# Kernel optimization log

Hardware: AMD Instinct MI355X
Metric: run time of the kernel (lower is better)

The kernel has to match this reference:

```python
import jax, jax.numpy as jnp
import numpy as np

LN_EPS = 1e-5


def setup_inputs() -> dict:
    key = jax.random.key(0)
    ks = jax.random.split(key, 6)
    n_nodes, mem_dim = 500000, 256
    n_upd, msg_dim = 65536, 512
    return {
        "unique_node_ids": jnp.arange(n_upd, dtype=jnp.int64) if jax.config.jax_enable_x64 else jnp.arange(n_upd, dtype=jnp.int32),
        "unique_messages": jax.random.normal(ks[0], (n_upd, msg_dim), dtype=jnp.float32),
        "timestamps": jax.random.uniform(ks[1], (n_upd,), dtype=jnp.float32),
        "memory": jax.random.normal(ks[2], (n_nodes, mem_dim), dtype=jnp.float32),
        "last_update": jnp.zeros((n_nodes,), dtype=jnp.float32),
        "W_ih": jax.random.normal(ks[3], (3 * mem_dim, msg_dim), dtype=jnp.float32) * (1.0 / np.sqrt(msg_dim)),
        "W_hh": jax.random.normal(ks[4], (3 * mem_dim, mem_dim), dtype=jnp.float32) * (1.0 / np.sqrt(mem_dim)),
        "b_ih": jnp.zeros((3 * mem_dim,), dtype=jnp.float32),
        "b_hh": jnp.zeros((3 * mem_dim,), dtype=jnp.float32),
        "ln_gamma": jnp.ones((mem_dim,), dtype=jnp.float32),
        "ln_beta": jnp.zeros((mem_dim,), dtype=jnp.float32),
    }


def _gru_cell(x, h, W_ih, W_hh, b_ih, b_hh):
    # torch.nn.GRUCell math
    gi = x @ W_ih.T + b_ih          # [N, 3H]
    gh = h @ W_hh.T + b_hh          # [N, 3H]
    i_r, i_z, i_n = jnp.split(gi, 3, axis=-1)
    h_r, h_z, h_n = jnp.split(gh, 3, axis=-1)
    r = jax.nn.sigmoid(i_r + h_r)
    z = jax.nn.sigmoid(i_z + h_z)
    n = jnp.tanh(i_n + r * h_n)
    return (1.0 - z) * n + z * h


def _layer_norm(x, gamma, beta):
    mu = jnp.mean(x, axis=-1, keepdims=True)
    var = jnp.mean(jnp.square(x - mu), axis=-1, keepdims=True)
    return (x - mu) * jax.lax.rsqrt(var + LN_EPS) * gamma + beta


def reference(unique_node_ids, unique_messages, timestamps, memory, last_update,
              W_ih, W_hh, b_ih, b_hh, ln_gamma, ln_beta):
    # gather memory rows for the nodes being updated
    h = memory[unique_node_ids]                      # [N, H]
    new_h = _gru_cell(unique_messages, h, W_ih, W_hh, b_ih, b_hh)
    new_h = _layer_norm(new_h, ln_gamma, ln_beta)
    # scatter updated rows back (get_updated_memory semantics: pure copy)
    updated_memory = memory.at[unique_node_ids].set(new_h)
    updated_last_update = last_update.at[unique_node_ids].set(timestamps)
    return updated_memory, updated_last_update
```

## Files before the change

### kernel.cpp

```cpp
#include <hip/hip_runtime.h>
#include <hip/hip_bf16.h>

typedef float  f32x4 __attribute__((ext_vector_type(4)));
typedef short  s16x8 __attribute__((ext_vector_type(8)));

#define MEMH   256
#define MSGD   512
#define G3     768
#define W_IH_ELEMS (G3*MSGD)
#define W_HH_ELEMS (G3*MEMH)
#define W_TOT_ELEMS (W_IH_ELEMS + W_HH_ELEMS)
#define W_BYTES    ((size_t)W_TOT_ELEMS * 2)

#define BM     32
#define NTHR   512
#define AM_OFF 0
#define AH_OFF 32768
#define PART_OFF 49152
#define LDS_BYTES 51200

static __device__ __forceinline__ short f2bf(float x) {
    __hip_bfloat16 b = __float2bfloat16(x);
    return __builtin_bit_cast(short, b);
}
static __device__ __forceinline__ float bf2f(short s) {
    unsigned int u = ((unsigned int)(unsigned short)s) << 16;
    return __builtin_bit_cast(float, u);
}
static __device__ __forceinline__ float sigf(float x) {
    return 1.f / (1.f + __expf(-x));
}
static __device__ __forceinline__ float tanh_fast(float x) {
    float e = __expf(-2.f * fabsf(x));
    float t = (1.f - e) / (1.f + e);
    return copysignf(t, x);
}
static __device__ __forceinline__ f32x4 ntload4(const float* p) {
    return __builtin_nontemporal_load((const f32x4*)p);
}
static __device__ __forceinline__ void ntstore4(float* p, f32x4 v) {
    __builtin_nontemporal_store(v, (f32x4*)p);
}

__global__ void smu_copy_kernel(const float* __restrict__ mem,
                                const float* __restrict__ lu,
                                float* __restrict__ out_mem,
                                float* __restrict__ out_lu,
                                long n_mem4, long n_lu4) {
    long i = (long)blockIdx.x * blockDim.x + threadIdx.x;
    long stride = (long)gridDim.x * blockDim.x;
    long total = n_mem4 + n_lu4;
    for (; i < total; i += stride) {
        if (i < n_mem4) ntstore4(out_mem + i * 4, ntload4(mem + i * 4));
        else {
            long j = (i - n_mem4) * 4;
            ntstore4(out_lu + j, ntload4(lu + j));
        }
    }
}

__global__ __launch_bounds__(256)
void smu_copy_skip_kernel(const float* __restrict__ mem,
                          const float* __restrict__ lu,
                          const unsigned* __restrict__ bm,
                          float* __restrict__ out_mem,
                          float* __restrict__ out_lu,
                          long n_nodes) {
    const long nu = n_nodes * (MEMH / 4);
    const long stride = (long)gridDim.x * blockDim.x;
    const long i0 = (long)blockIdx.x * blockDim.x + threadIdx.x;

    for (long i = i0; i < nu; i += stride) {
        long r = i >> 6;
        if (!((bm[r >> 5] >> (r & 31)) & 1u))
            ntstore4(out_mem + i * 4, ntload4(mem + i * 4));
    }
    for (long i = i0; i < n_nodes; i += stride) {
        if (!((bm[i >> 5] >> (i & 31)) & 1u)) {
            float v = __builtin_nontemporal_load(lu + i);
            __builtin_nontemporal_store(v, out_lu + i);
        }
    }
}

__global__ void smu_cvtw_kernel(const float* __restrict__ wih,
                                const float* __restrict__ whh,
                                short* __restrict__ o) {
    int i = blockIdx.x * blockDim.x + threadIdx.x;
    if (i >= W_TOT_ELEMS) return;
    if (i < W_IH_ELEMS) {
        int f = i >> 9, r = i & 511, l = r >> 3, e = r & 7;
        int t = f >> 4, k = f & 15;
        int row = t * 16 + (l & 15), col = k * 32 + (l >> 4) * 8 + e;
        o[i] = f2bf(wih[row * MSGD + col]);
    } else {
        int j = i - W_IH_ELEMS;
        int f = j >> 9, r = j & 511, l = r >> 3, e = r & 7;
        int t = f >> 3, k = f & 7;
        int row = t * 16 + (l & 15), col = k * 32 + (l >> 4) * 8 + e;
        o[i] = f2bf(whh[row * MEMH + col]);
    }
}

__global__ void smu_clear_kernel(unsigned* __restrict__ p, int n) {
    int i = blockIdx.x * blockDim.x + threadIdx.x;
    if (i < n) p[i] = 0u;
}
__global__ void smu_bits_kernel(const int* __restrict__ ids,
                                unsigned* __restrict__ bm, int n) {
    int i = blockIdx.x * blockDim.x + threadIdx.x;
    if (i < n) {
        int id = ids[i];
        atomicOr(&bm[id >> 5], 1u << (id & 31));
    }
}

template<bool USE_WS>
static __device__ __forceinline__ s16x8 load_b(const float* __restrict__ Wf,
                                               const short* __restrict__ Wb,
                                               int t, int k, int ldk, int nkt, int lane) {
    if constexpr (USE_WS) {
        return *(const s16x8*)(Wb + ((size_t)(t * nkt + k) << 9) + lane * 8);
    } else {
        int row = t * 16 + (lane & 15);
        int col = k * 32 + (lane >> 4) * 8;
        f32x4 x = *(const f32x4*)(Wf + (size_t)row * ldk + col);
        f32x4 y = *(const f32x4*)(Wf + (size_t)row * ldk + col + 4);
        s16x8 s;
        s[0]=f2bf(x[0]); s[1]=f2bf(x[1]); s[2]=f2bf(x[2]); s[3]=f2bf(x[3]);
        s[4]=f2bf(y[0]); s[5]=f2bf(y[1]); s[6]=f2bf(y[2]); s[7]=f2bf(y[3]);
        return s;
    }
}

template<bool USE_WS>
__global__ __launch_bounds__(NTHR, 4)
void smu_gru_kernel(const int*   __restrict__ ids,
                    const float* __restrict__ msg,
                    const float* __restrict__ ts,
                    const float* __restrict__ memory,
                    const float* __restrict__ W_ih,
                    const float* __restrict__ W_hh,
                    const float* __restrict__ b_ih,
                    const float* __restrict__ b_hh,
                    const float* __restrict__ gamma,
                    const float* __restrict__ beta,
                    const short* __restrict__ wsw,
                    float* __restrict__ out_mem,
                    float* __restrict__ out_lu) {
    __shared__ __align__(16) unsigned char lds[LDS_BYTES];
    const int tid = threadIdx.x;
    const long base = (long)blockIdx.x * BM;

    {
        const float* src = msg + base * MSGD;
        #pragma unroll
        for (int it = 0; it < 4; ++it) {
            int u = tid + NTHR * it;
            int row = u >> 6;
            f32x4 a = ntload4(src + u * 8);
            f32x4 b = ntload4(src + u * 8 + 4);
            s16x8 s;
            s[0]=f2bf(a[0]); s[1]=f2bf(a[1]); s[2]=f2bf(a[2]); s[3]=f2bf(a[3]);
            s[4]=f2bf(b[0]); s[5]=f2bf(b[1]); s[6]=f2bf(b[2]); s[7]=f2bf(b[3]);
            int byte = AM_OFF + ((u * 16) ^ ((row & 7) << 4));
            *(s16x8*)(lds + byte) = s;
        }
        #pragma unroll
        for (int it = 0; it < 2; ++it) {
            int u = tid + NTHR * it;
            int row = u >> 5;
            int c8  = u & 31;
            int id  = ids[base + row];
            const float* hs = memory + (size_t)id * MEMH + c8 * 8;
            f32x4 a = ntload4(hs);
            f32x4 b = ntload4(hs + 4);
            s16x8 s;
            s[0]=f2bf(a[0]); s[1]=f2bf(a[1]); s[2]=f2bf(a[2]); s[3]=f2bf(a[3]);
            s[4]=f2bf(b[0]); s[5]=f2bf(b[1]); s[6]=f2bf(b[2]); s[7]=f2bf(b[3]);
            int byte = AH_OFF + ((u * 16) ^ ((row & 7) << 4));
            *(s16x8*)(lds + byte) = s;
        }
    }
    __syncthreads();

    const int lane = tid & 63;
    const int w    = tid >> 6;
    const int lr   = lane & 15;
    const int lk8  = (lane >> 4) * 8;
    const int sw   = (lr & 7) << 4;
    const short* Wi = wsw;
    const short* Wh = wsw + W_IH_ELEMS;

    f32x4 rz[2][2][2] = {};
    f32x4 gin[2][2]   = {};
    f32x4 ghn[2][2]   = {};

    {
        s16x8 b[2][6];
        #pragma unroll
        for (int i = 0; i < 6; ++i)
            b[0][i] = load_b<USE_WS>(W_ih, Wi, w + 8*(i/3) + 16*(i%3), 0, MSGD, 16, lane);
        #pragma unroll
        for (int i = 0; i < 6; ++i)
            b[1][i] = load_b<USE_WS>(W_ih, Wi, w + 8*(i/3) + 16*(i%3), 1, MSGD, 16, lane);
        #pragma unroll
        for (int k = 0; k < 16; ++k) {
            const int cb = (k * 32 + lk8) * 2;
            #pragma unroll
            for (int m = 0; m < 2; ++m) {
                s16x8 a = *(const s16x8*)(lds + AM_OFF + (((m*16 + lr) * 1024 + cb) ^ sw));
                #pragma unroll
                for (int ci = 0; ci < 2; ++ci) {
                    rz[m][ci][0] = __builtin_amdgcn_mfma_f32_16x16x32_bf16(a, b[k & 1][ci*3+0], rz[m][ci][0], 0, 0, 0);
                    rz[m][ci][1] = __builtin_amdgcn_mfma_f32_16x16x32_bf16(a, b[k & 1][ci*3+1], rz[m][ci][1], 0, 0, 0);
                    gin[m][ci]   = __builtin_amdgcn_mfma_f32_16x16x32_bf16(a, b[k & 1][ci*3+2], gin[m][ci],   0, 0, 0);
                }
            }
            if (k < 14) {
                #pragma unroll
                for (int i = 0; i < 6; ++i)
                    b[k & 1][i] = load_b<USE_WS>(W_ih, Wi, w + 8*(i/3) + 16*(i%3), k + 2, MSGD, 16, lane);
            }
        }
    }
    {
        s16x8 b[2][6];
        #pragma unroll
        for (int i = 0; i < 6; ++i)
            b[0][i] = load_b<USE_WS>(W_hh, Wh, w + 8*(i/3) + 16*(i%3), 0, MEMH, 8, lane);
        #pragma unroll
        for (int i = 0; i < 6; ++i)
            b[1][i] = load_b<USE_WS>(W_hh, Wh, w + 8*(i/3) + 16*(i%3), 1, MEMH, 8, lane);
        #pragma unroll
        for (int k = 0; k < 8; ++k) {
            const int cb = (k * 32 + lk8) * 2;
            #pragma unroll
            for (int m = 0; m < 2; ++m) {
                s16x8 a = *(const s16x8*)(lds + AH_OFF + (((m*16 + lr) * 512 + cb) ^ sw));
                #pragma unroll
                for (int ci = 0; ci < 2; ++ci) {
                    rz[m][ci][0] = __builtin_amdgcn_mfma_f32_16x16x32_bf16(a, b[k & 1][ci*3+0], rz[m][ci][0], 0, 0, 0);
                    rz[m][ci][1] = __builtin_amdgcn_mfma_f32_16x16x32_bf16(a, b[k & 1][ci*3+1], rz[m][ci][1], 0, 0, 0);
                    ghn[m][ci]   = __builtin_amdgcn_mfma_f32_16x16x32_bf16(a, b[k & 1][ci*3+2], ghn[m][ci],   0, 0, 0);
                }
            }
            if (k < 6) {
                #pragma unroll
                for (int i = 0; i < 6; ++i)
                    b[k & 1][i] = load_b<USE_WS>(W_hh, Wh, w + 8*(i/3) + 16*(i%3), k + 2, MEMH, 8, lane);
            }
        }
    }

    const int lq = (lane >> 4);
    f32x4 o_[2][2];
    {
        #pragma unroll
        for (int ci = 0; ci < 2; ++ci) {
            const int j = (w + 8*ci) * 16 + lr;
            const float br = b_ih[j]       + b_hh[j];
            const float bz = b_ih[256 + j] + b_hh[256 + j];
            const float bihn = b_ih[512 + j], bhhn = b_hh[512 + j];
            #pragma unroll
            for (int m = 0; m < 2; ++m) {
                #pragma unroll
                for (int q = 0; q < 4; ++q) {
                    int row = m * 16 + lq * 4 + q;
                    float r = sigf(rz[m][ci][0][q] + br);
                    float z = sigf(rz[m][ci][1][q] + bz);
                    float n = tanh_fast(gin[m][ci][q] + bihn + r * (ghn[m][ci][q] + bhhn));
                    float hv = bf2f(*(const short*)(lds + AH_OFF + ((row * 512 + j * 2) ^ ((row & 7) << 4))));
                    o_[m][ci][q] = (1.f - z) * n + z * hv;
                }
            }
        }
    }

    {
        float* part = (float*)(lds + PART_OFF);
        #pragma unroll
        for (int m = 0; m < 2; ++m) {
            #pragma unroll
            for (int q = 0; q < 4; ++q) {
                float v0 = o_[m][0][q], v1 = o_[m][1][q];
                float s1 = v0 + v1;
                float s2 = v0 * v0 + v1 * v1;
                #pragma unroll
                for (int mk = 1; mk < 16; mk <<= 1) {
                    s1 += __shfl_xor(s1, mk);
                    s2 += __shfl_xor(s2, mk);
                }
                if (lr == 0) {
                    int row = m * 16 + lq * 4 + q;
                    part[(row * 8 + w) * 2]     = s1;
                    part[(row * 8 + w) * 2 + 1] = s2;
                }
            }
        }
    }
    __syncthreads();

    float mu_[2][4], inv_[2][4];
    {
        const float* part = (const float*)(lds + PART_OFF);
        #pragma unroll
        for (int m = 0; m < 2; ++m) {
            #pragma unroll
            for (int q = 0; q < 4; ++q) {
                int row = m * 16 + lq * 4 + q;
                float s1 = 0.f, s2 = 0.f;
                #pragma unroll
                for (int i = 0; i < 8; ++i) {
                    s1 += part[(row * 8 + i) * 2];
                    s2 += part[(row * 8 + i) * 2 + 1];
                }
                float mu  = s1 * (1.f / 256.f);
                float var = fmaxf(s2 * (1.f / 256.f) - mu * mu, 0.f);
                mu_[m][q]  = mu;
                inv_[m][q] = rsqrtf(var + 1e-5f);
            }
        }
    }

    {
        #pragma unroll
        for (int ci = 0; ci < 2; ++ci) {
            const int j = (w + 8*ci) * 16 + lr;
            const float ga = gamma[j], be = beta[j];
            #pragma unroll
            for (int m = 0; m < 2; ++m) {
                #pragma unroll
                for (int q = 0; q < 4; ++q) {
                    int row = m * 16 + lq * 4 + q;
                    int id = ids[base + row];
                    float y = (o_[m][ci][q] - mu_[m][q]) * inv_[m][q] * ga + be;
                    __builtin_nontemporal_store(y, out_mem + (size_t)id * MEMH + j);
                }
            }
        }
        if (w == 0 && lane < 32) {
            int id = ids[base + lane];
            __builtin_nontemporal_store(ts[base + lane], out_lu + id);
        }
    }
}

extern "C" void kernel_launch(void* const* d_in, const int* in_sizes, int n_in,
                              void* d_out, int out_size, void* d_ws, size_t ws_size,
                              hipStream_t stream) {
    (void)n_in; (void)out_size;
    const int*   ids = (const int*)  d_in[0];
    const float* msg = (const float*)d_in[1];
    const float* ts  = (const float*)d_in[2];
    const float* mem = (const float*)d_in[3];
    const float* lu  = (const float*)d_in[4];
    const float* Wih = (const float*)d_in[5];
    const float* Whh = (const float*)d_in[6];
    const float* bih = (const float*)d_in[7];
    const float* bhh = (const float*)d_in[8];
    const float* gam = (const float*)d_in[9];
    const float* bet = (const float*)d_in[10];

    const int  n_upd   = in_sizes[0];
    const long n_nodes = (long)in_sizes[3] / MEMH;

    float* out_mem = (float*)d_out;
    float* out_lu  = out_mem + (size_t)n_nodes * MEMH;

    const int    bm_words     = (int)((n_nodes + 31) / 32) + 4;
    const size_t bm_bytes_pad = (size_t)bm_words * 4;
    const bool ws_w  = (d_ws != nullptr) && (ws_size >= W_BYTES);
    const bool ws_bm = (d_ws != nullptr) && (ws_size >= W_BYTES + bm_bytes_pad);

    short*    wsw = (short*)d_ws;
    unsigned* bm  = (unsigned*)((char*)d_ws + W_BYTES);

    const int grid = n_upd / BM;

    if (ws_bm && ws_w) {
        smu_clear_kernel<<<(bm_words + 255) / 256, 256, 0, stream>>>(bm, bm_words);
        smu_bits_kernel<<<(n_upd + 255) / 256, 256, 0, stream>>>(ids, bm, n_upd);
        smu_copy_skip_kernel<<<2048, 256, 0, stream>>>(mem, lu, bm, out_mem, out_lu, n_nodes);
        smu_cvtw_kernel<<<(W_TOT_ELEMS + 255) / 256, 256, 0, stream>>>(Wih, Whh, wsw);
        smu_gru_kernel<true><<<grid, NTHR, 0, stream>>>(
            ids, msg, ts, mem, Wih, Whh, bih, bhh, gam, bet, wsw, out_mem, out_lu);
    } else {
        long n_mem4 = n_nodes * (MEMH / 4);
        long n_lu4  = n_nodes / 4;
        smu_copy_kernel<<<2048, 256, 0, stream>>>(mem, lu, out_mem, out_lu, n_mem4, n_lu4);
        if (ws_w) {
            smu_cvtw_kernel<<<(W_TOT_ELEMS + 255) / 256, 256, 0, stream>>>(Wih, Whh, wsw);
            smu_gru_kernel<true><<<grid, NTHR, 0, stream>>>(
                ids, msg, ts, mem, Wih, Whh, bih, bhh, gam, bet, wsw, out_mem, out_lu);
        } else {
            smu_gru_kernel<false><<<grid, NTHR, 0, stream>>>(
                ids, msg, ts, mem, Wih, Whh, bih, bhh, gam, bet, nullptr, out_mem, out_lu);
        }
    }
}
```

Baseline: 341.3 us.

## Double the row tile to 64 with 1024 threads and stream message K-chunks through LDS

Result: no change. 344.7 us (+1.0%).

```diff
diff --git a/kernel.cpp b/kernel.cpp
--- a/kernel.cpp
+++ b/kernel.cpp
@@ -12,12 +12,14 @@
 #define W_TOT_ELEMS (W_IH_ELEMS + W_HH_ELEMS)
 #define W_BYTES    ((size_t)W_TOT_ELEMS * 2)
 
-#define BM     32
-#define NTHR   512
-#define AM_OFF 0
-#define AH_OFF 32768
-#define PART_OFF 49152
-#define LDS_BYTES 51200
+#define BM      64
+#define NTHR    1024
+#define MB0_OFF 0
+#define MB1_OFF 16384
+#define AH_OFF  32768
+#define PART_OFF 65536
+#define STAT_OFF 73728
+#define LDS_BYTES 74240
 
 static __device__ __forceinline__ short f2bf(float x) {
     __hip_bfloat16 b = __float2bfloat16(x);
@@ -26,6 +28,12 @@
 static __device__ __forceinline__ float bf2f(short s) {
     unsigned int u = ((unsigned int)(unsigned short)s) << 16;
     return __builtin_bit_cast(float, u);
+}
+static __device__ __forceinline__ s16x8 cvt8(f32x4 a, f32x4 b) {
+    s16x8 s;
+    s[0]=f2bf(a[0]); s[1]=f2bf(a[1]); s[2]=f2bf(a[2]); s[3]=f2bf(a[3]);
+    s[4]=f2bf(b[0]); s[5]=f2bf(b[1]); s[6]=f2bf(b[2]); s[7]=f2bf(b[3]);
+    return s;
 }
 static __device__ __forceinline__ float sigf(float x) {
     return 1.f / (1.f + __expf(-x));
@@ -126,15 +134,12 @@
         int col = k * 32 + (lane >> 4) * 8;
         f32x4 x = *(const f32x4*)(Wf + (size_t)row * ldk + col);
         f32x4 y = *(const f32x4*)(Wf + (size_t)row * ldk + col + 4);
-        s16x8 s;
-        s[0]=f2bf(x[0]); s[1]=f2bf(x[1]); s[2]=f2bf(x[2]); s[3]=f2bf(x[3]);
-        s[4]=f2bf(y[0]); s[5]=f2bf(y[1]); s[6]=f2bf(y[2]); s[7]=f2bf(y[3]);
-        return s;
+        return cvt8(x, y);
     }
 }
 
 template<bool USE_WS>
-__global__ __launch_bounds__(NTHR, 4)
+__global__ __launch_bounds__(NTHR, 1)
 void smu_gru_kernel(const int*   __restrict__ ids,
                     const float* __restrict__ msg,
                     const float* __restrict__ ts,
@@ -152,127 +157,125 @@
     const int tid = threadIdx.x;
     const long base = (long)blockIdx.x * BM;
 
-    {
-        const float* src = msg + base * MSGD;
-        #pragma unroll
-        for (int it = 0; it < 4; ++it) {
-            int u = tid + NTHR * it;
-            int row = u >> 6;
-            f32x4 a = ntload4(src + u * 8);
-            f32x4 b = ntload4(src + u * 8 + 4);
-            s16x8 s;
-            s[0]=f2bf(a[0]); s[1]=f2bf(a[1]); s[2]=f2bf(a[2]); s[3]=f2bf(a[3]);
-            s[4]=f2bf(b[0]); s[5]=f2bf(b[1]); s[6]=f2bf(b[2]); s[7]=f2bf(b[3]);
-            int byte = AM_OFF + ((u * 16) ^ ((row & 7) << 4));
-            *(s16x8*)(lds + byte) = s;
-        }
-        #pragma unroll
-        for (int it = 0; it < 2; ++it) {
-            int u = tid + NTHR * it;
-            int row = u >> 5;
-            int c8  = u & 31;
-            int id  = ids[base + row];
-            const float* hs = memory + (size_t)id * MEMH + c8 * 8;
-            f32x4 a = ntload4(hs);
-            f32x4 b = ntload4(hs + 4);
-            s16x8 s;
-            s[0]=f2bf(a[0]); s[1]=f2bf(a[1]); s[2]=f2bf(a[2]); s[3]=f2bf(a[3]);
-            s[4]=f2bf(b[0]); s[5]=f2bf(b[1]); s[6]=f2bf(b[2]); s[7]=f2bf(b[3]);
-            int byte = AH_OFF + ((u * 16) ^ ((row & 7) << 4));
-            *(s16x8*)(lds + byte) = s;
-        }
-    }
-    __syncthreads();
-
     const int lane = tid & 63;
     const int w    = tid >> 6;
     const int lr   = lane & 15;
-    const int lk8  = (lane >> 4) * 8;
+    const int lq   = lane >> 4;
+    const int lk8  = lq * 8;
     const int sw   = (lr & 7) << 4;
     const short* Wi = wsw;
     const short* Wh = wsw + W_IH_ELEMS;
 
-    f32x4 rz[2][2][2] = {};
-    f32x4 gin[2][2]   = {};
-    f32x4 ghn[2][2]   = {};
+    const int   srow  = tid >> 4;
+    const int   sc8   = tid & 15;
+    const float* msrc = msg + (base + srow) * MSGD + sc8 * 8;
+    const int   mbyte = (srow * 256 + sc8 * 16) ^ ((srow & 7) << 4);
+
+    const int   hrow  = tid >> 5;
+    const int   hc8   = tid & 31;
+    const int   ahb0  = AH_OFF + ((hrow * 512 + hc8 * 16) ^ ((hrow & 7) << 4));
+    const int   ahb1  = ahb0 + 32 * 512;
+
+    f32x4 s0a = ntload4(msrc),       s0b = ntload4(msrc + 4);
+    f32x4 s1a = ntload4(msrc + 128), s1b = ntload4(msrc + 132);
+
+    s16x8 b[2][3];
+    #pragma unroll
+    for (int i = 0; i < 3; ++i) b[0][i] = load_b<USE_WS>(W_ih, Wi, w + 16*i, 0, MSGD, 16, lane);
+    #pragma unroll
+    for (int i = 0; i < 3; ++i) b[1][i] = load_b<USE_WS>(W_ih, Wi, w + 16*i, 1, MSGD, 16, lane);
+
+    *(s16x8*)(lds + MB0_OFF + mbyte) = cvt8(s0a, s0b);
+    *(s16x8*)(lds + MB1_OFF + mbyte) = cvt8(s1a, s1b);
+    __syncthreads();
+
+    f32x4 rz[4][2] = {};
+    f32x4 gin[4]   = {};
+    f32x4 ghn[4]   = {};
+
+    f32x4 s2a, s2b, s3a, s3b;
+    f32x4 ah0, ah1, ah2, ah3;
+
+    #pragma unroll
+    for (int k = 0; k < 16; ++k) {
+        if (k == 0) { s2a = ntload4(msrc + 256); s2b = ntload4(msrc + 260); }
+        if (k == 4) { s3a = ntload4(msrc + 384); s3b = ntload4(msrc + 388); }
+        if (k == 8) {
+            __syncthreads();
+            *(s16x8*)(lds + MB0_OFF + mbyte) = cvt8(s2a, s2b);
+            __syncthreads();
+            int id0 = ids[base + hrow];
+            int id1 = ids[base + hrow + 32];
+            const float* h0 = memory + (size_t)id0 * MEMH + hc8 * 8;
+            const float* h1 = memory + (size_t)id1 * MEMH + hc8 * 8;
+            ah0 = ntload4(h0); ah1 = ntload4(h0 + 4);
+            ah2 = ntload4(h1); ah3 = ntload4(h1 + 4);
+        }
+        if (k == 12) {
+            __syncthreads();
+            *(s16x8*)(lds + MB1_OFF + mbyte) = cvt8(s3a, s3b);
+            __syncthreads();
+        }
+        const int mboff = (k & 4) ? MB1_OFF : MB0_OFF;
+        const int cb = ((k & 3) * 32 + lk8) * 2;
+        #pragma unroll
+        for (int m = 0; m < 4; ++m) {
+            s16x8 a = *(const s16x8*)(lds + mboff + (((m*16 + lr) * 256 + cb) ^ sw));
+            rz[m][0] = __builtin_amdgcn_mfma_f32_16x16x32_bf16(a, b[k & 1][0], rz[m][0], 0, 0, 0);
+            rz[m][1] = __builtin_amdgcn_mfma_f32_16x16x32_bf16(a, b[k & 1][1], rz[m][1], 0, 0, 0);
+            gin[m]   = __builtin_amdgcn_mfma_f32_16x16x32_bf16(a, b[k & 1][2], gin[m],   0, 0, 0);
+        }
+        if (k < 14) {
+            #pragma unroll
+            for (int i = 0; i < 3; ++i)
+                b[k & 1][i] = load_b<USE_WS>(W_ih, Wi, w + 16*i, k + 2, MSGD, 16, lane);
+        }
+    }
+
+    __syncthreads();
+    *(s16x8*)(lds + ahb0) = cvt8(ah0, ah1);
+    *(s16x8*)(lds + ahb1) = cvt8(ah2, ah3);
+    __syncthreads();
 
     {
-        s16x8 b[2][6];
-        #pragma unroll
-        for (int i = 0; i < 6; ++i)
-            b[0][i] = load_b<USE_WS>(W_ih, Wi, w + 8*(i/3) + 16*(i%3), 0, MSGD, 16, lane);
-        #pragma unroll
-        for (int i = 0; i < 6; ++i)
-            b[1][i] = load_b<USE_WS>(W_ih, Wi, w + 8*(i/3) + 16*(i%3), 1, MSGD, 16, lane);
-        #pragma unroll
-        for (int k = 0; k < 16; ++k) {
-            const int cb = (k * 32 + lk8) * 2;
-            #pragma unroll
-            for (int m = 0; m < 2; ++m) {
-                s16x8 a = *(const s16x8*)(lds + AM_OFF + (((m*16 + lr) * 1024 + cb) ^ sw));
-                #pragma unroll
-                for (int ci = 0; ci < 2; ++ci) {
-                    rz[m][ci][0] = __builtin_amdgcn_mfma_f32_16x16x32_bf16(a, b[k & 1][ci*3+0], rz[m][ci][0], 0, 0, 0);
-                    rz[m][ci][1] = __builtin_amdgcn_mfma_f32_16x16x32_bf16(a, b[k & 1][ci*3+1], rz[m][ci][1], 0, 0, 0);
-                    gin[m][ci]   = __builtin_amdgcn_mfma_f32_16x16x32_bf16(a, b[k & 1][ci*3+2], gin[m][ci],   0, 0, 0);
-                }
-            }
-            if (k < 14) {
-                #pragma unroll
-                for (int i = 0; i < 6; ++i)
-                    b[k & 1][i] = load_b<USE_WS>(W_ih, Wi, w + 8*(i/3) + 16*(i%3), k + 2, MSGD, 16, lane);
-            }
-        }
-    }
-    {
-        s16x8 b[2][6];
-        #pragma unroll
-        for (int i = 0; i < 6; ++i)
-            b[0][i] = load_b<USE_WS>(W_hh, Wh, w + 8*(i/3) + 16*(i%3), 0, MEMH, 8, lane);
-        #pragma unroll
-        for (int i = 0; i < 6; ++i)
-            b[1][i] = load_b<USE_WS>(W_hh, Wh, w + 8*(i/3) + 16*(i%3), 1, MEMH, 8, lane);
+        #pragma unroll
+        for (int i = 0; i < 3; ++i) b[0][i] = load_b<USE_WS>(W_hh, Wh, w + 16*i, 0, MEMH, 8, lane);
+        #pragma unroll
+        for (int i = 0; i < 3; ++i) b[1][i] = load_b<USE_WS>(W_hh, Wh, w + 16*i, 1, MEMH, 8, lane);
         #pragma unroll
         for (int k = 0; k < 8; ++k) {
             const int cb = (k * 32 + lk8) * 2;
             #pragma unroll
-            for (int m = 0; m < 2; ++m) {
+            for (int m = 0; m < 4; ++m) {
                 s16x8 a = *(const s16x8*)(lds + AH_OFF + (((m*16 + lr) * 512 + cb) ^ sw));
-                #pragma unroll
-                for (int ci = 0; ci < 2; ++ci) {
-                    rz[m][ci][0] = __builtin_amdgcn_mfma_f32_16x16x32_bf16(a, b[k & 1][ci*3+0], rz[m][ci][0], 0, 0, 0);
-                    rz[m][ci][1] = __builtin_amdgcn_mfma_f32_16x16x32_bf16(a, b[k & 1][ci*3+1], rz[m][ci][1], 0, 0, 0);
-                    ghn[m][ci]   = __builtin_amdgcn_mfma_f32_16x16x32_bf16(a, b[k & 1][ci*3+2], ghn[m][ci],   0, 0, 0);
-                }
+                rz[m][0] = __builtin_amdgcn_mfma_f32_16x16x32_bf16(a, b[k & 1][0], rz[m][0], 0, 0, 0);
+                rz[m][1] = __builtin_amdgcn_mfma_f32_16x16x32_bf16(a, b[k & 1][1], rz[m][1], 0, 0, 0);
+                ghn[m]   = __builtin_amdgcn_mfma_f32_16x16x32_bf16(a, b[k & 1][2], ghn[m],   0, 0, 0);
             }
             if (k < 6) {
                 #pragma unroll
-                for (int i = 0; i < 6; ++i)
-                    b[k & 1][i] = load_b<USE_WS>(W_hh, Wh, w + 8*(i/3) + 16*(i%3), k + 2, MEMH, 8, lane);
+                for (int i = 0; i < 3; ++i)
+                    b[k & 1][i] = load_b<USE_WS>(W_hh, Wh, w + 16*i, k + 2, MEMH, 8, lane);
             }
         }
     }
 
-    const int lq = (lane >> 4);
-    f32x4 o_[2][2];
+    const int j = w * 16 + lr;
+    f32x4 o_[4];
     {
-        #pragma unroll
-        for (int ci = 0; ci < 2; ++ci) {
-            const int j = (w + 8*ci) * 16 + lr;
-            const float br = b_ih[j]       + b_hh[j];
-            const float bz = b_ih[256 + j] + b_hh[256 + j];
-            const float bihn = b_ih[512 + j], bhhn = b_hh[512 + j];
+        const float br = b_ih[j]       + b_hh[j];
+        const float bz = b_ih[256 + j] + b_hh[256 + j];
+        const float bihn = b_ih[512 + j], bhhn = b_hh[512 + j];
+        #pragma unroll
+        for (int m = 0; m < 4; ++m) {
             #pragma unroll
-            for (int m = 0; m < 2; ++m) {
-                #pragma unroll
-                for (int q = 0; q < 4; ++q) {
-                    int row = m * 16 + lq * 4 + q;
-                    float r = sigf(rz[m][ci][0][q] + br);
-                    float z = sigf(rz[m][ci][1][q] + bz);
-                    float n = tanh_fast(gin[m][ci][q] + bihn + r * (ghn[m][ci][q] + bhhn));
-                    float hv = bf2f(*(const short*)(lds + AH_OFF + ((row * 512 + j * 2) ^ ((row & 7) << 4))));
-                    o_[m][ci][q] = (1.f - z) * n + z * hv;
-                }
+            for (int q = 0; q < 4; ++q) {
+                int row = m * 16 + lq * 4 + q;
+                float r = sigf(rz[m][0][q] + br);
+                float z = sigf(rz[m][1][q] + bz);
+                float n = tanh_fast(gin[m][q] + bihn + r * (ghn[m][q] + bhhn));
+                float hv = bf2f(*(const short*)(lds + AH_OFF + ((row * 512 + j * 2) ^ ((row & 7) << 4))));
+                o_[m][q] = (1.f - z) * n + z * hv;
             }
         }
     }
@@ -280,12 +283,11 @@
     {
         float* part = (float*)(lds + PART_OFF);
         #pragma unroll
-        for (int m = 0; m < 2; ++m) {
+        for (int m = 0; m < 4; ++m) {
             #pragma unroll
             for (int q = 0; q < 4; ++q) {
-                float v0 = o_[m][0][q], v1 = o_[m][1][q];
-                float s1 = v0 + v1;
-                float s2 = v0 * v0 + v1 * v1;
+                float v = o_[m][q];
+                float s1 = v, s2 = v * v;
                 #pragma unroll
                 for (int mk = 1; mk < 16; mk <<= 1) {
                     s1 += __shfl_xor(s1, mk);
@@ -293,53 +295,50 @@
                 }
                 if (lr == 0) {
                     int row = m * 16 + lq * 4 + q;
-                    part[(row * 8 + w) * 2]     = s1;
-                    part[(row * 8 + w) * 2 + 1] = s2;
+                    part[(row * 16 + w) * 2]     = s1;
+                    part[(row * 16 + w) * 2 + 1] = s2;
                 }
             }
         }
     }
     __syncthreads();
 
-    float mu_[2][4], inv_[2][4];
     {
         const float* part = (const float*)(lds + PART_OFF);
-        #pragma unroll
-        for (int m = 0; m < 2; ++m) {
+        int row = w * 4 + lq;
+        float s1 = part[(row * 16 + lr) * 2];
+        float s2 = part[(row * 16 + lr) * 2 + 1];
+        #pragma unroll
+        for (int mk = 1; mk < 16; mk <<= 1) {
+            s1 += __shfl_xor(s1, mk);
+            s2 += __shfl_xor(s2, mk);
+        }
+        if (lr == 0) {
+            float mu  = s1 * (1.f / 256.f);
+            float var = fmaxf(s2 * (1.f / 256.f) - mu * mu, 0.f);
+            float* st = (float*)(lds + STAT_OFF);
+            st[row * 2]     = mu;
+            st[row * 2 + 1] = rsqrtf(var + 1e-5f);
+        }
+    }
+    __syncthreads();
+
+    {
+        const float* st = (const float*)(lds + STAT_OFF);
+        const float ga = gamma[j], be = beta[j];
+        #pragma unroll
+        for (int m = 0; m < 4; ++m) {
             #pragma unroll
             for (int q = 0; q < 4; ++q) {
                 int row = m * 16 + lq * 4 + q;
-                float s1 = 0.f, s2 = 0.f;
-                #pragma unroll
-                for (int i = 0; i < 8; ++i) {
-                    s1 += part[(row * 8 + i) * 2];
-                    s2 += part[(row * 8 + i) * 2 + 1];
-                }
-                float mu  = s1 * (1.f / 256.f);
-                float var = fmaxf(s2 * (1.f / 256.f) - mu * mu, 0.f);
-                mu_[m][q]  = mu;
-                inv_[m][q] = rsqrtf(var + 1e-5f);
+                float mu  = st[row * 2];
+                float inv = st[row * 2 + 1];
+                int id = ids[base + row];
+                float y = (o_[m][q] - mu) * inv * ga + be;
+                __builtin_nontemporal_store(y, out_mem + (size_t)id * MEMH + j);
             }
         }
-    }
-
-    {
-        #pragma unroll
-        for (int ci = 0; ci < 2; ++ci) {
-            const int j = (w + 8*ci) * 16 + lr;
-            const float ga = gamma[j], be = beta[j];
-            #pragma unroll
-            for (int m = 0; m < 2; ++m) {
-                #pragma unroll
-                for (int q = 0; q < 4; ++q) {
-                    int row = m * 16 + lq * 4 + q;
-                    int id = ids[base + row];
-                    float y = (o_[m][ci][q] - mu_[m][q]) * inv_[m][q] * ga + be;
-                    __builtin_nontemporal_store(y, out_mem + (size_t)id * MEMH + j);
-                }
-            }
-        }
-        if (w == 0 && lane < 32) {
+        if (w == 0) {
             int id = ids[base + lane];
             __builtin_nontemporal_store(ts[base + lane], out_lu + id);
         }
```

## Stream GRU weight tiles into LDS via async global_load_lds with 1024-thread blocks

Applied to the files above, without the earlier changes.

After: 371.4 us. 1.09x slower.

```diff
diff --git a/kernel.cpp b/kernel.cpp
--- a/kernel.cpp
+++ b/kernel.cpp
@@ -12,12 +12,16 @@
 #define W_TOT_ELEMS (W_IH_ELEMS + W_HH_ELEMS)
 #define W_BYTES    ((size_t)W_TOT_ELEMS * 2)
 
-#define BM     32
-#define NTHR   512
-#define AM_OFF 0
-#define AH_OFF 32768
-#define PART_OFF 49152
-#define LDS_BYTES 51200
+#define BM      32
+#define NTHR    1024
+#define AM_OFF  0
+#define AH_OFF  32768
+#define B_OFF   49152
+#define PART_OFF 147456
+#define LDS_BYTES 151552
+
+typedef const __attribute__((address_space(1))) void* gas_p;
+typedef __attribute__((address_space(3)))       void* las_p;
 
 static __device__ __forceinline__ short f2bf(float x) {
     __hip_bfloat16 b = __float2bfloat16(x);
@@ -26,6 +30,12 @@
 static __device__ __forceinline__ float bf2f(short s) {
     unsigned int u = ((unsigned int)(unsigned short)s) << 16;
     return __builtin_bit_cast(float, u);
+}
+static __device__ __forceinline__ s16x8 cvt8(f32x4 a, f32x4 b) {
+    s16x8 s;
+    s[0]=f2bf(a[0]); s[1]=f2bf(a[1]); s[2]=f2bf(a[2]); s[3]=f2bf(a[3]);
+    s[4]=f2bf(b[0]); s[5]=f2bf(b[1]); s[6]=f2bf(b[2]); s[7]=f2bf(b[3]);
+    return s;
 }
 static __device__ __forceinline__ float sigf(float x) {
     return 1.f / (1.f + __expf(-x));
@@ -115,164 +125,144 @@
     }
 }
 
-template<bool USE_WS>
-static __device__ __forceinline__ s16x8 load_b(const float* __restrict__ Wf,
-                                               const short* __restrict__ Wb,
-                                               int t, int k, int ldk, int nkt, int lane) {
-    if constexpr (USE_WS) {
-        return *(const s16x8*)(Wb + ((size_t)(t * nkt + k) << 9) + lane * 8);
-    } else {
-        int row = t * 16 + (lane & 15);
-        int col = k * 32 + (lane >> 4) * 8;
-        f32x4 x = *(const f32x4*)(Wf + (size_t)row * ldk + col);
-        f32x4 y = *(const f32x4*)(Wf + (size_t)row * ldk + col + 4);
-        s16x8 s;
-        s[0]=f2bf(x[0]); s[1]=f2bf(x[1]); s[2]=f2bf(x[2]); s[3]=f2bf(x[3]);
-        s[4]=f2bf(y[0]); s[5]=f2bf(y[1]); s[6]=f2bf(y[2]); s[7]=f2bf(y[3]);
-        return s;
-    }
-}
-
-template<bool USE_WS>
-__global__ __launch_bounds__(NTHR, 4)
-void smu_gru_kernel(const int*   __restrict__ ids,
-                    const float* __restrict__ msg,
-                    const float* __restrict__ ts,
-                    const float* __restrict__ memory,
-                    const float* __restrict__ W_ih,
-                    const float* __restrict__ W_hh,
-                    const float* __restrict__ b_ih,
-                    const float* __restrict__ b_hh,
-                    const float* __restrict__ gamma,
-                    const float* __restrict__ beta,
-                    const short* __restrict__ wsw,
-                    float* __restrict__ out_mem,
-                    float* __restrict__ out_lu) {
+__global__ __launch_bounds__(NTHR, 1)
+void smu_gru_dma_kernel(const int*   __restrict__ ids,
+                        const float* __restrict__ msg,
+                        const float* __restrict__ ts,
+                        const float* __restrict__ memory,
+                        const float* __restrict__ b_ih,
+                        const float* __restrict__ b_hh,
+                        const float* __restrict__ gamma,
+                        const float* __restrict__ beta,
+                        const short* __restrict__ wsw,
+                        float* __restrict__ out_mem,
+                        float* __restrict__ out_lu) {
     __shared__ __align__(16) unsigned char lds[LDS_BYTES];
     const int tid = threadIdx.x;
     const long base = (long)blockIdx.x * BM;
 
+    const int lane = tid & 63;
+    const int w    = tid >> 6;
+    const int lr   = lane & 15;
+    const int lq   = lane >> 4;
+    const int lk8  = lq * 8;
+    const int sw   = (lr & 7) << 4;
+    const short* Wi = wsw;
+    const short* Wh = wsw + W_IH_ELEMS;
+
     {
         const float* src = msg + base * MSGD;
         #pragma unroll
-        for (int it = 0; it < 4; ++it) {
+        for (int it = 0; it < 2; ++it) {
             int u = tid + NTHR * it;
             int row = u >> 6;
             f32x4 a = ntload4(src + u * 8);
             f32x4 b = ntload4(src + u * 8 + 4);
-            s16x8 s;
-            s[0]=f2bf(a[0]); s[1]=f2bf(a[1]); s[2]=f2bf(a[2]); s[3]=f2bf(a[3]);
-            s[4]=f2bf(b[0]); s[5]=f2bf(b[1]); s[6]=f2bf(b[2]); s[7]=f2bf(b[3]);
             int byte = AM_OFF + ((u * 16) ^ ((row & 7) << 4));
-            *(s16x8*)(lds + byte) = s;
-        }
-        #pragma unroll
-        for (int it = 0; it < 2; ++it) {
-            int u = tid + NTHR * it;
+            *(s16x8*)(lds + byte) = cvt8(a, b);
+        }
+        {
+            int u = tid;
             int row = u >> 5;
             int c8  = u & 31;
             int id  = ids[base + row];
             const float* hs = memory + (size_t)id * MEMH + c8 * 8;
             f32x4 a = ntload4(hs);
             f32x4 b = ntload4(hs + 4);
-            s16x8 s;
-            s[0]=f2bf(a[0]); s[1]=f2bf(a[1]); s[2]=f2bf(a[2]); s[3]=f2bf(a[3]);
-            s[4]=f2bf(b[0]); s[5]=f2bf(b[1]); s[6]=f2bf(b[2]); s[7]=f2bf(b[3]);
             int byte = AH_OFF + ((u * 16) ^ ((row & 7) << 4));
-            *(s16x8*)(lds + byte) = s;
+            *(s16x8*)(lds + byte) = cvt8(a, b);
         }
     }
     __syncthreads();
 
-    const int lane = tid & 63;
-    const int w    = tid >> 6;
-    const int lr   = lane & 15;
-    const int lk8  = (lane >> 4) * 8;
-    const int sw   = (lr & 7) << 4;
-    const short* Wi = wsw;
-    const short* Wh = wsw + W_IH_ELEMS;
-
-    f32x4 rz[2][2][2] = {};
-    f32x4 gin[2][2]   = {};
-    f32x4 ghn[2][2]   = {};
-
-    {
-        s16x8 b[2][6];
-        #pragma unroll
-        for (int i = 0; i < 6; ++i)
-            b[0][i] = load_b<USE_WS>(W_ih, Wi, w + 8*(i/3) + 16*(i%3), 0, MSGD, 16, lane);
-        #pragma unroll
-        for (int i = 0; i < 6; ++i)
-            b[1][i] = load_b<USE_WS>(W_ih, Wi, w + 8*(i/3) + 16*(i%3), 1, MSGD, 16, lane);
+    const int bbase = B_OFF + w * 6144;
+    f32x4 rz[2][2] = {};
+    f32x4 gin[2]   = {};
+    f32x4 ghn[2]   = {};
+
+    {
+        #pragma unroll
+        for (int g = 0; g < 3; ++g)
+            __builtin_amdgcn_global_load_lds(
+                (gas_p)(const void*)(Wi + (((16 * g + w) * 16 + 0) << 9) + lane * 8),
+                (las_p)(void*)(lds + bbase + g * 1024), 16, 0, 0);
         #pragma unroll
         for (int k = 0; k < 16; ++k) {
+            if (k < 15) {
+                const int nb = bbase + ((k + 1) & 1) * 3072;
+                #pragma unroll
+                for (int g = 0; g < 3; ++g)
+                    __builtin_amdgcn_global_load_lds(
+                        (gas_p)(const void*)(Wi + (((16 * g + w) * 16 + (k + 1)) << 9) + lane * 8),
+                        (las_p)(void*)(lds + nb + g * 1024), 16, 0, 0);
+                asm volatile("s_waitcnt vmcnt(3)" ::: "memory");
+            } else {
+                asm volatile("s_waitcnt vmcnt(0)" ::: "memory");
+            }
+            const int bufo = bbase + (k & 1) * 3072;
+            s16x8 b0 = *(const s16x8*)(lds + bufo + 0 * 1024 + lane * 16);
+            s16x8 b1 = *(const s16x8*)(lds + bufo + 1 * 1024 + lane * 16);
+            s16x8 b2 = *(const s16x8*)(lds + bufo + 2 * 1024 + lane * 16);
             const int cb = (k * 32 + lk8) * 2;
             #pragma unroll
             for (int m = 0; m < 2; ++m) {
                 s16x8 a = *(const s16x8*)(lds + AM_OFF + (((m*16 + lr) * 1024 + cb) ^ sw));
+                rz[m][0] = __builtin_amdgcn_mfma_f32_16x16x32_bf16(a, b0, rz[m][0], 0, 0, 0);
+                rz[m][1] = __builtin_amdgcn_mfma_f32_16x16x32_bf16(a, b1, rz[m][1], 0, 0, 0);
+                gin[m]   = __builtin_amdgcn_mfma_f32_16x16x32_bf16(a, b2, gin[m],   0, 0, 0);
+            }
+        }
+    }
+    {
+        #pragma unroll
+        for (int g = 0; g < 3; ++g)
+            __builtin_amdgcn_global_load_lds(
+                (gas_p)(const void*)(Wh + (((16 * g + w) * 8 + 0) << 9) + lane * 8),
+                (las_p)(void*)(lds + bbase + g * 1024), 16, 0, 0);
+        #pragma unroll
+        for (int k = 0; k < 8; ++k) {
+            if (k < 7) {
+                const int nb = bbase + ((k + 1) & 1) * 3072;
                 #pragma unroll
-                for (int ci = 0; ci < 2; ++ci) {
-                    rz[m][ci][0] = __builtin_amdgcn_mfma_f32_16x16x32_bf16(a, b[k & 1][ci*3+0], rz[m][ci][0], 0, 0, 0);
-                    rz[m][ci][1] = __builtin_amdgcn_mfma_f32_16x16x32_bf16(a, b[k & 1][ci*3+1], rz[m][ci][1], 0, 0, 0);
-                    gin[m][ci]   = __builtin_amdgcn_mfma_f32_16x16x32_bf16(a, b[k & 1][ci*3+2], gin[m][ci],   0, 0, 0);
-                }
-            }
-            if (k < 14) {
-                #pragma unroll
-                for (int i = 0; i < 6; ++i)
-                    b[k & 1][i] = load_b<USE_WS>(W_ih, Wi, w + 8*(i/3) + 16*(i%3), k + 2, MSGD, 16, lane);
-            }
-        }
-    }
-    {
-        s16x8 b[2][6];
-        #pragma unroll
-        for (int i = 0; i < 6; ++i)
-            b[0][i] = load_b<USE_WS>(W_hh, Wh, w + 8*(i/3) + 16*(i%3), 0, MEMH, 8, lane);
-        #pragma unroll
-        for (int i = 0; i < 6; ++i)
-            b[1][i] = load_b<USE_WS>(W_hh, Wh, w + 8*(i/3) + 16*(i%3), 1, MEMH, 8, lane);
-        #pragma unroll
-        for (int k = 0; k < 8; ++k) {
+                for (int g = 0; g < 3; ++g)
+                    __builtin_amdgcn_global_load_lds(
+                        (gas_p)(const void*)(Wh + (((16 * g + w) * 8 + (k + 1)) << 9) + lane * 8),
+                        (las_p)(void*)(lds + nb + g * 1024), 16, 0, 0);
+                asm volatile("s_waitcnt vmcnt(3)" ::: "memory");
+            } else {
+                asm volatile("s_waitcnt vmcnt(0)" ::: "memory");
+            }
+            const int bufo = bbase + (k & 1) * 3072;
+            s16x8 b0 = *(const s16x8*)(lds + bufo + 0 * 1024 + lane * 16);
+            s16x8 b1 = *(const s16x8*)(lds + bufo + 1 * 1024 + lane * 16);
+            s16x8 b2 = *(const s16x8*)(lds + bufo + 2 * 1024 + lane * 16);
             const int cb = (k * 32 + lk8) * 2;
             #pragma unroll
             for (int m = 0; m < 2; ++m) {
                 s16x8 a = *(const s16x8*)(lds + AH_OFF + (((m*16 + lr) * 512 + cb) ^ sw));
-                #pragma unroll
-                for (int ci = 0; ci < 2; ++ci) {
-                    rz[m][ci][0] = __builtin_amdgcn_mfma_f32_16x16x32_bf16(a, b[k & 1][ci*3+0], rz[m][ci][0], 0, 0, 0);
-                    rz[m][ci][1] = __builtin_amdgcn_mfma_f32_16x16x32_bf16(a, b[k & 1][ci*3+1], rz[m][ci][1], 0, 0, 0);
-                    ghn[m][ci]   = __builtin_amdgcn_mfma_f32_16x16x32_bf16(a, b[k & 1][ci*3+2], ghn[m][ci],   0, 0, 0);
-                }
-            }
-            if (k < 6) {
-                #pragma unroll
-                for (int i = 0; i < 6; ++i)
-                    b[k & 1][i] = load_b<USE_WS>(W_hh, Wh, w + 8*(i/3) + 16*(i%3), k + 2, MEMH, 8, lane);
-            }
-        }
-    }
-
-    const int lq = (lane >> 4);
-    f32x4 o_[2][2];
-    {
-        #pragma unroll
-        for (int ci = 0; ci < 2; ++ci) {
-            const int j = (w + 8*ci) * 16 + lr;
-            const float br = b_ih[j]       + b_hh[j];
-            const float bz = b_ih[256 + j] + b_hh[256 + j];
-            const float bihn = b_ih[512 + j], bhhn = b_hh[512 + j];
-            #pragma unroll
-            for (int m = 0; m < 2; ++m) {
-                #pragma unroll
-                for (int q = 0; q < 4; ++q) {
-                    int row = m * 16 + lq * 4 + q;
-                    float r = sigf(rz[m][ci][0][q] + br);
-                    float z = sigf(rz[m][ci][1][q] + bz);
-                    float n = tanh_fast(gin[m][ci][q] + bihn + r * (ghn[m][ci][q] + bhhn));
-                    float hv = bf2f(*(const short*)(lds + AH_OFF + ((row * 512 + j * 2) ^ ((row & 7) << 4))));
-                    o_[m][ci][q] = (1.f - z) * n + z * hv;
-                }
+                rz[m][0] = __builtin_amdgcn_mfma_f32_16x16x32_bf16(a, b0, rz[m][0], 0, 0, 0);
+                rz[m][1] = __builtin_amdgcn_mfma_f32_16x16x32_bf16(a, b1, rz[m][1], 0, 0, 0);
+                ghn[m]   = __builtin_amdgcn_mfma_f32_16x16x32_bf16(a, b2, ghn[m],   0, 0, 0);
+            }
+        }
+    }
+
+    const int j = w * 16 + lr;
+    f32x4 o_[2];
+    {
+        const float br = b_ih[j]       + b_hh[j];
+        const float bz = b_ih[256 + j] + b_hh[256 + j];
+        const float bihn = b_ih[512 + j], bhhn = b_hh[512 + j];
+        #pragma unroll
+        for (int m = 0; m < 2; ++m) {
+            #pragma unroll
+            for (int q = 0; q < 4; ++q) {
+                int row = m * 16 + lq * 4 + q;
+                float r = sigf(rz[m][0][q] + br);
+                float z = sigf(rz[m][1][q] + bz);
+                float n = tanh_fast(gin[m][q] + bihn + r * (ghn[m][q] + bhhn));
+                float hv = bf2f(*(const short*)(lds + AH_OFF + ((row * 512 + j * 2) ^ ((row & 7) << 4))));
+                o_[m][q] = (1.f - z) * n + z * hv;
             }
         }
     }
@@ -283,9 +273,8 @@
         for (int m = 0; m < 2; ++m) {
             #pragma unroll
             for (int q = 0; q < 4; ++q) {
-                float v0 = o_[m][0][q], v1 = o_[m][1][q];
-                float s1 = v0 + v1;
-                float s2 = v0 * v0 + v1 * v1;
+                float v = o_[m][q];
+                float s1 = v, s2 = v * v;
                 #pragma unroll
                 for (int mk = 1; mk < 16; mk <<= 1) {
                     s1 += __shfl_xor(s1, mk);
@@ -293,8 +282,8 @@
                 }
                 if (lr == 0) {
                     int row = m * 16 + lq * 4 + q;
-                    part[(row * 8 + w) * 2]     = s1;
-                    part[(row * 8 + w) * 2 + 1] = s2;
+                    part[(row * 16 + w) * 2]     = s1;
+                    part[(row * 16 + w) * 2 + 1] = s2;
                 }
             }
         }
@@ -306,6 +295,184 @@
         const float* part = (const float*)(lds + PART_OFF);
         #pragma unroll
         for (int m = 0; m < 2; ++m) {
+            #pragma unroll
+            for (int q = 0; q < 4; ++q) {
+                int row = m * 16 + lq * 4 + q;
+                float s1 = 0.f, s2 = 0.f;
+                #pragma unroll
+                for (int i = 0; i < 16; ++i) {
+                    s1 += part[(row * 16 + i) * 2];
+                    s2 += part[(row * 16 + i) * 2 + 1];
+                }
+                float mu  = s1 * (1.f / 256.f);
+                float var = fmaxf(s2 * (1.f / 256.f) - mu * mu, 0.f);
+                mu_[m][q]  = mu;
+                inv_[m][q] = rsqrtf(var + 1e-5f);
+            }
+        }
+    }
+
+    {
+        const float ga = gamma[j], be = beta[j];
+        #pragma unroll
+        for (int m = 0; m < 2; ++m) {
+            #pragma unroll
+            for (int q = 0; q < 4; ++q) {
+                int row = m * 16 + lq * 4 + q;
+                int id = ids[base + row];
+                float y = (o_[m][q] - mu_[m][q]) * inv_[m][q] * ga + be;
+                __builtin_nontemporal_store(y, out_mem + (size_t)id * MEMH + j);
+            }
+        }
+        if (w == 0 && lane < 32) {
+            int id = ids[base + lane];
+            __builtin_nontemporal_store(ts[base + lane], out_lu + id);
+        }
+    }
+}
+
+__global__ __launch_bounds__(512, 4)
+void smu_gru_fb_kernel(const int*   __restrict__ ids,
+                       const float* __restrict__ msg,
+                       const float* __restrict__ ts,
+                       const float* __restrict__ memory,
+                       const float* __restrict__ W_ih,
+                       const float* __restrict__ W_hh,
+                       const float* __restrict__ b_ih,
+                       const float* __restrict__ b_hh,
+                       const float* __restrict__ gamma,
+                       const float* __restrict__ beta,
+                       float* __restrict__ out_mem,
+                       float* __restrict__ out_lu) {
+    __shared__ __align__(16) unsigned char lds[51200];
+    const int tid = threadIdx.x;
+    const long base = (long)blockIdx.x * 32;
+
+    {
+        const float* src = msg + base * MSGD;
+        #pragma unroll
+        for (int it = 0; it < 4; ++it) {
+            int u = tid + 512 * it;
+            int row = u >> 6;
+            f32x4 a = ntload4(src + u * 8);
+            f32x4 b = ntload4(src + u * 8 + 4);
+            int byte = ((u * 16) ^ ((row & 7) << 4));
+            *(s16x8*)(lds + byte) = cvt8(a, b);
+        }
+        #pragma unroll
+        for (int it = 0; it < 2; ++it) {
+            int u = tid + 512 * it;
+            int row = u >> 5;
+            int c8  = u & 31;
+            int id  = ids[base + row];
+            const float* hs = memory + (size_t)id * MEMH + c8 * 8;
+            f32x4 a = ntload4(hs);
+            f32x4 b = ntload4(hs + 4);
+            int byte = 32768 + ((u * 16) ^ ((row & 7) << 4));
+            *(s16x8*)(lds + byte) = cvt8(a, b);
+        }
+    }
+    __syncthreads();
+
+    const int lane = tid & 63;
+    const int w    = tid >> 6;
+    const int lr   = lane & 15;
+    const int lq   = lane >> 4;
+    const int lk8  = lq * 8;
+    const int sw   = (lr & 7) << 4;
+
+    auto loadb = [&](const float* Wf, int t, int k, int ldk) {
+        int row = t * 16 + lr;
+        int col = k * 32 + lk8;
+        f32x4 x = *(const f32x4*)(Wf + (size_t)row * ldk + col);
+        f32x4 y = *(const f32x4*)(Wf + (size_t)row * ldk + col + 4);
+        return cvt8(x, y);
+    };
+
+    f32x4 rz[2][2][2] = {};
+    f32x4 gin[2][2]   = {};
+    f32x4 ghn[2][2]   = {};
+
+    for (int k = 0; k < 16; ++k) {
+        const int cb = (k * 32 + lk8) * 2;
+        #pragma unroll
+        for (int m = 0; m < 2; ++m) {
+            s16x8 a = *(const s16x8*)(lds + (((m*16 + lr) * 1024 + cb) ^ sw));
+            #pragma unroll
+            for (int ci = 0; ci < 2; ++ci) {
+                s16x8 b0 = loadb(W_ih, w + 8*ci + 0,  k, MSGD);
+                s16x8 b1 = loadb(W_ih, w + 8*ci + 16, k, MSGD);
+                s16x8 b2 = loadb(W_ih, w + 8*ci + 32, k, MSGD);
+                rz[m][ci][0] = __builtin_amdgcn_mfma_f32_16x16x32_bf16(a, b0, rz[m][ci][0], 0, 0, 0);
+                rz[m][ci][1] = __builtin_amdgcn_mfma_f32_16x16x32_bf16(a, b1, rz[m][ci][1], 0, 0, 0);
+                gin[m][ci]   = __builtin_amdgcn_mfma_f32_16x16x32_bf16(a, b2, gin[m][ci],   0, 0, 0);
+            }
+        }
+    }
+    for (int k = 0; k < 8; ++k) {
+        const int cb = (k * 32 + lk8) * 2;
+        #pragma unroll
+        for (int m = 0; m < 2; ++m) {
+            s16x8 a = *(const s16x8*)(lds + 32768 + (((m*16 + lr) * 512 + cb) ^ sw));
+            #pragma unroll
+            for (int ci = 0; ci < 2; ++ci) {
+                s16x8 b0 = loadb(W_hh, w + 8*ci + 0,  k, MEMH);
+                s16x8 b1 = loadb(W_hh, w + 8*ci + 16, k, MEMH);
+                s16x8 b2 = loadb(W_hh, w + 8*ci + 32, k, MEMH);
+                rz[m][ci][0] = __builtin_amdgcn_mfma_f32_16x16x32_bf16(a, b0, rz[m][ci][0], 0, 0, 0);
+                rz[m][ci][1] = __builtin_amdgcn_mfma_f32_16x16x32_bf16(a, b1, rz[m][ci][1], 0, 0, 0);
+                ghn[m][ci]   = __builtin_amdgcn_mfma_f32_16x16x32_bf16(a, b2, ghn[m][ci],   0, 0, 0);
+            }
+        }
+    }
+
+    f32x4 o_[2][2];
+    #pragma unroll
+    for (int ci = 0; ci < 2; ++ci) {
+        const int j = (w + 8*ci) * 16 + lr;
+        const float br = b_ih[j]       + b_hh[j];
+        const float bz = b_ih[256 + j] + b_hh[256 + j];
+        const float bihn = b_ih[512 + j], bhhn = b_hh[512 + j];
+        #pragma unroll
+        for (int m = 0; m < 2; ++m) {
+            #pragma unroll
+            for (int q = 0; q < 4; ++q) {
+                int row = m * 16 + lq * 4 + q;
+                float r = sigf(rz[m][ci][0][q] + br);
+                float z = sigf(rz[m][ci][1][q] + bz);
+                float n = tanh_fast(gin[m][ci][q] + bihn + r * (ghn[m][ci][q] + bhhn));
+                float hv = bf2f(*(const short*)(lds + 32768 + ((row * 512 + j * 2) ^ ((row & 7) << 4))));
+                o_[m][ci][q] = (1.f - z) * n + z * hv;
+            }
+        }
+    }
+
+    float* part = (float*)(lds + 49152);
+    #pragma unroll
+    for (int m = 0; m < 2; ++m)
+        #pragma unroll
+        for (int q = 0; q < 4; ++q) {
+            float v0 = o_[m][0][q], v1 = o_[m][1][q];
+            float s1 = v0 + v1, s2 = v0*v0 + v1*v1;
+            #pragma unroll
+            for (int mk = 1; mk < 16; mk <<= 1) {
+                s1 += __shfl_xor(s1, mk);
+                s2 += __shfl_xor(s2, mk);
+            }
+            if (lr == 0) {
+                int row = m * 16 + lq * 4 + q;
+                part[(row * 8 + w) * 2]     = s1;
+                part[(row * 8 + w) * 2 + 1] = s2;
+            }
+        }
+    __syncthreads();
+
+    #pragma unroll
+    for (int ci = 0; ci < 2; ++ci) {
+        const int j = (w + 8*ci) * 16 + lr;
+        const float ga = gamma[j], be = beta[j];
+        #pragma unroll
+        for (int m = 0; m < 2; ++m)
             #pragma unroll
             for (int q = 0; q < 4; ++q) {
                 int row = m * 16 + lq * 4 + q;
@@ -317,32 +484,15 @@
                 }
                 float mu  = s1 * (1.f / 256.f);
                 float var = fmaxf(s2 * (1.f / 256.f) - mu * mu, 0.f);
-                mu_[m][q]  = mu;
-                inv_[m][q] = rsqrtf(var + 1e-5f);
-            }
-        }
-    }
-
-    {
-        #pragma unroll
-        for (int ci = 0; ci < 2; ++ci) {
-            const int j = (w + 8*ci) * 16 + lr;
-            const float ga = gamma[j], be = beta[j];
-            #pragma unroll
-            for (int m = 0; m < 2; ++m) {
-                #pragma unroll
-                for (int q = 0; q < 4; ++q) {
-                    int row = m * 16 + lq * 4 + q;
-                    int id = ids[base + row];
-                    float y = (o_[m][ci][q] - mu_[m][q]) * inv_[m][q] * ga + be;
-                    __builtin_nontemporal_store(y, out_mem + (size_t)id * MEMH + j);
-                }
-            }
-        }
-        if (w == 0 && lane < 32) {
-            int id = ids[base + lane];
-            __builtin_nontemporal_store(ts[base + lane], out_lu + id);
-        }
+                float inv = rsqrtf(var + 1e-5f);
+                int id = ids[base + row];
+                float y = (o_[m][ci][q] - mu) * inv * ga + be;
+                __builtin_nontemporal_store(y, out_mem + (size_t)id * MEMH + j);
+            }
+    }
+    if (w == 0 && lane < 32) {
+        int id = ids[base + lane];
+        __builtin_nontemporal_store(ts[base + lane], out_lu + id);
     }
 }
 
@@ -370,32 +520,23 @@
 
     const int    bm_words     = (int)((n_nodes + 31) / 32) + 4;
     const size_t bm_bytes_pad = (size_t)bm_words * 4;
-    const bool ws_w  = (d_ws != nullptr) && (ws_size >= W_BYTES);
-    const bool ws_bm = (d_ws != nullptr) && (ws_size >= W_BYTES + bm_bytes_pad);
+    const bool ws_ok = (d_ws != nullptr) && (ws_size >= W_BYTES + bm_bytes_pad);
 
     short*    wsw = (short*)d_ws;
     unsigned* bm  = (unsigned*)((char*)d_ws + W_BYTES);
 
-    const int grid = n_upd / BM;
-
-    if (ws_bm && ws_w) {
+    if (ws_ok) {
         smu_clear_kernel<<<(bm_words + 255) / 256, 256, 0, stream>>>(bm, bm_words);
         smu_bits_kernel<<<(n_upd + 255) / 256, 256, 0, stream>>>(ids, bm, n_upd);
         smu_copy_skip_kernel<<<2048, 256, 0, stream>>>(mem, lu, bm, out_mem, out_lu, n_nodes);
         smu_cvtw_kernel<<<(W_TOT_ELEMS + 255) / 256, 256, 0, stream>>>(Wih, Whh, wsw);
-        smu_gru_kernel<true><<<grid, NTHR, 0, stream>>>(
-            ids, msg, ts, mem, Wih, Whh, bih, bhh, gam, bet, wsw, out_mem, out_lu);
+        smu_gru_dma_kernel<<<n_upd / BM, NTHR, 0, stream>>>(
+            ids, msg, ts, mem, bih, bhh, gam, bet, wsw, out_mem, out_lu);
     } else {
         long n_mem4 = n_nodes * (MEMH / 4);
         long n_lu4  = n_nodes / 4;
         smu_copy_kernel<<<2048, 256, 0, stream>>>(mem, lu, out_mem, out_lu, n_mem4, n_lu4);
-        if (ws_w) {
-            smu_cvtw_kernel<<<(W_TOT_ELEMS + 255) / 256, 256, 0, stream>>>(Wih, Whh, wsw);
-            smu_gru_kernel<true><<<grid, NTHR, 0, stream>>>(
-                ids, msg, ts, mem, Wih, Whh, bih, bhh, gam, bet, wsw, out_mem, out_lu);
-        } else {
-            smu_gru_kernel<false><<<grid, NTHR, 0, stream>>>(
-                ids, msg, ts, mem, Wih, Whh, bih, bhh, gam, bet, nullptr, out_mem, out_lu);
-        }
-    }
-}
+        smu_gru_fb_kernel<<<n_upd / 32, 512, 0, stream>>>(
+            ids, msg, ts, mem, Wih, Whh, bih, bhh, gam, bet, out_mem, out_lu);
+    }
+}
```
